# Performance work log

Hardware: AMD Instinct MI355X
Metric: run time of the kernel (lower is better)

The kernel has to match this reference:

```python
import jax, jax.numpy as jnp
import numpy as np

DIM = 1024
N_HEADS = 16
HEAD_DIM = DIM // N_HEADS


def setup_inputs() -> dict:
    key = jax.random.key(0)
    ks = jax.random.split(key, 9)
    s = 0.02
    return {
        "x": jax.random.normal(ks[0], (2, 2048, DIM), dtype=jnp.float32),
        "Wq": jax.random.normal(ks[1], (DIM, DIM), dtype=jnp.float32) * s,
        "bq": jax.random.normal(ks[2], (DIM,), dtype=jnp.float32) * s,
        "Wk": jax.random.normal(ks[3], (DIM, DIM), dtype=jnp.float32) * s,
        "bk": jax.random.normal(ks[4], (DIM,), dtype=jnp.float32) * s,
        "Wv": jax.random.normal(ks[5], (DIM, DIM), dtype=jnp.float32) * s,
        "bv": jax.random.normal(ks[6], (DIM,), dtype=jnp.float32) * s,
        "Wo": jax.random.normal(ks[7], (DIM, DIM), dtype=jnp.float32) * s,
        "bo": jax.random.normal(ks[8], (DIM,), dtype=jnp.float32) * s,
    }


def reference(x, Wq, bq, Wk, bk, Wv, bv, Wo, bo):
    B, T, C = x.shape
    # QKV projections, split heads -> [B, H, T, D]
    def split_heads(t):
        return t.reshape(B, T, N_HEADS, HEAD_DIM).transpose(0, 2, 1, 3)
    q = split_heads(x @ Wq + bq)
    k = split_heads(x @ Wk + bk)
    v = split_heads(x @ Wv + bv)
    scale = 1.0 / jnp.sqrt(jnp.float32(HEAD_DIM))
    scores = jnp.einsum("bhqd,bhkd->bhqk", q, k) * scale  # [B,H,T,T]
    causal = jnp.tril(jnp.ones((T, T), dtype=bool))  # True = keep
    scores = jnp.where(causal, scores, jnp.float32(-jnp.inf))
    weights = jax.nn.softmax(scores, axis=-1)
    ctx = jnp.einsum("bhqk,bhkd->bhqd", weights, v)
    ctx = ctx.transpose(0, 2, 1, 3).reshape(B, T, C)
    return ctx @ Wo + bo
```

## Files before the change

### kernel.cpp

```cpp
#include <hip/hip_runtime.h>
#include <hip/hip_bf16.h>
#include <stdint.h>

#define DIM    1024
#define SEQ    2048
#define NB     2
#define NH     16
#define HD     64
#define NROWS  (NB*SEQ)

typedef unsigned short u16;
typedef __attribute__((ext_vector_type(8))) short bf16x8;
typedef __attribute__((ext_vector_type(4))) float f32x4;
typedef __attribute__((ext_vector_type(4))) unsigned short u16x4;

#define NEG_INF (-__builtin_inff())

__device__ __forceinline__ u16 f2bf(float f) {
    union { float f; uint32_t u; } x; x.f = f;
    uint32_t r = x.u + 0x7FFFu + ((x.u >> 16) & 1u);
    return (u16)(r >> 16);
}

__device__ __forceinline__ uint32_t cvtpk(float a, float b) {
    uint32_t r;
    asm volatile("v_cvt_pk_bf16_f32 %0, %1, %2" : "=v"(r) : "v"(a), "v"(b));
    return r;
}

__device__ __forceinline__ void gload_lds16(const void* g, void* l) {
    __builtin_amdgcn_global_load_lds(
        (const __attribute__((address_space(1))) void*)g,
        (__attribute__((address_space(3))) void*)l, 16, 0, 0);
}

__global__ __launch_bounds__(256)
void cvt_x(const float* __restrict__ in, u16* __restrict__ out)
{
    size_t i = (size_t)blockIdx.x * 256 + threadIdx.x;
    float4 f = *(const float4*)&in[i * 4];
    u16x4 o = { f2bf(f.x), f2bf(f.y), f2bf(f.z), f2bf(f.w) };
    *(u16x4*)&out[i * 4] = o;
}

__global__ __launch_bounds__(256)
void cvt_w(const float* __restrict__ Wq, const float* __restrict__ Wk,
           const float* __restrict__ Wv, const float* __restrict__ Wo,
           u16* __restrict__ Wqt, u16* __restrict__ Wkt,
           u16* __restrict__ Wvt, u16* __restrict__ Wot)
{
    __shared__ u16 Ws[64][68];
    const int z = blockIdx.z;
    const float* W = z == 0 ? Wq : z == 1 ? Wk : z == 2 ? Wv : Wo;
    u16* Wt        = z == 0 ? Wqt : z == 1 ? Wkt : z == 2 ? Wvt : Wot;
    const int k0 = blockIdx.x * 64;
    const int n0 = blockIdx.y * 64;
    const int tid = threadIdx.x;

    #pragma unroll
    for (int it = 0; it < 4; ++it) {
        int idx = tid + it * 256;
        int r = idx >> 4, cq = idx & 15;
        float4 f = *(const float4*)&W[(size_t)(k0 + r) * DIM + n0 + cq * 4];
        u16x4 o = { f2bf(f.x), f2bf(f.y), f2bf(f.z), f2bf(f.w) };
        *(u16x4*)&Ws[r][cq * 4] = o;
    }
    __syncthreads();
    #pragma unroll
    for (int it = 0; it < 4; ++it) {
        int idx = tid + it * 256;
        int rr = idx >> 4, cq = idx & 15;
        u16x4 o = { Ws[cq*4+0][rr], Ws[cq*4+1][rr], Ws[cq*4+2][rr], Ws[cq*4+3][rr] };
        *(u16x4*)&Wt[(size_t)(n0 + rr) * DIM + k0 + cq * 4] = o;
    }
}

template<int MODE, int BN>
__global__ __launch_bounds__(256)
void gemm_mfma(const u16* __restrict__ A,
               const u16* __restrict__ Wt0, const u16* __restrict__ Wt1,
               const u16* __restrict__ Wt2,
               const float* __restrict__ b0, const float* __restrict__ b1,
               const float* __restrict__ b2,
               void* __restrict__ o0, void* __restrict__ o1, void* __restrict__ o2)
{
    constexpr int NJ = BN / 32;
    __shared__ __align__(16) uint8_t lds[16384 + BN * 128];
    uint8_t* Asb = lds;
    uint8_t* Bsb = lds + 16384;

    const int tid  = threadIdx.x;
    const int wid  = tid >> 6, lane = tid & 63;
    const int lr   = lane & 15, lg = lane >> 4;
    const int wr   = wid >> 1, wc = wid & 1;

    const int r0 = blockIdx.x * 128;
    const int c0 = blockIdx.y * BN;

    const u16* Wt; const float* bias; u16* obf = nullptr; float* ofp = nullptr;
    int cw; float qscale = 1.0f;
    if (MODE == 0) {
        int sel = c0 >> 10;
        cw  = c0 & 1023;
        Wt   = sel == 0 ? Wt0 : sel == 1 ? Wt1 : Wt2;
        bias = sel == 0 ? b0  : sel == 1 ? b1  : b2;
        obf  = (u16*)(sel == 0 ? o0 : sel == 1 ? o1 : o2);
        if (sel == 0) qscale = 0.125f * 1.44269504088896f;
    } else {
        cw = c0; Wt = Wt0; bias = b0; ofp = (float*)o0;
    }

    f32x4 acc[4][NJ] = {};

    for (int k0 = 0; k0 < DIM; k0 += 64) {
        __syncthreads();
        #pragma unroll
        for (int seg = 0; seg < 4; ++seg) {
            int o   = seg * 4096 + tid * 16;
            int row = o >> 7;
            int sch = ((o >> 4) & 7) ^ (row & 7);
            gload_lds16((const uint8_t*)A  + ((size_t)(r0 + row) << 11) + (k0 << 1) + (sch << 4),
                        Asb + seg * 4096 + (wid << 10) + (lane << 4));
            if (seg < BN / 32)
                gload_lds16((const uint8_t*)Wt + ((size_t)(cw + row) << 11) + (k0 << 1) + (sch << 4),
                            Bsb + seg * 4096 + (wid << 10) + (lane << 4));
        }
        __syncthreads();

        __builtin_amdgcn_s_setprio(1);
        #pragma unroll
        for (int kk = 0; kk < 2; ++kk) {
            bf16x8 a[4], b[NJ];
            #pragma unroll
            for (int i = 0; i < 4; ++i) {
                int ar = wr * 64 + i * 16 + lr;
                a[i] = *(const bf16x8*)(Asb + ar * 128 + ((((kk << 2) | lg) ^ (ar & 7)) << 4));
            }
            #pragma unroll
            for (int j = 0; j < NJ; ++j) {
                int br = wc * (BN / 2) + j * 16 + lr;
                b[j] = *(const bf16x8*)(Bsb + br * 128 + ((((kk << 2) | lg) ^ (br & 7)) << 4));
            }
            #pragma unroll
            for (int i = 0; i < 4; ++i)
                #pragma unroll
                for (int j = 0; j < NJ; ++j)
                    acc[i][j] = __builtin_amdgcn_mfma_f32_16x16x32_bf16(a[i], b[j], acc[i][j], 0, 0, 0);
        }
        __builtin_amdgcn_s_setprio(0);
    }

    #pragma unroll
    for (int j = 0; j < NJ; ++j) {
        int colw = wc * (BN / 2) + j * 16 + lr;
        float bv = bias[cw + colw];
        #pragma unroll
        for (int i = 0; i < 4; ++i) {
            #pragma unroll
            for (int r = 0; r < 4; ++r) {
                float val = (acc[i][j][r] + bv) * qscale;
                int row = r0 + wr * 64 + i * 16 + lg * 4 + r;
                if (MODE == 0) {
                    int col = cw + colw;
                    int h = col >> 6, d = col & 63;
                    int bb = row >> 11, t = row & (SEQ - 1);
                    obf[((((size_t)bb * NH + h) * SEQ + t) << 6) + d] = f2bf(val);
                } else {
                    ofp[((size_t)row << 10) + c0 + colw] = val;
                }
            }
        }
    }
}

template<int SPLIT>
__global__ __launch_bounds__(256)
void attn_mfma(const u16* __restrict__ q, const u16* __restrict__ k,
               const u16* __restrict__ v, u16* __restrict__ ctx,
               float* __restrict__ pO, float* __restrict__ pML)
{
    __shared__ __align__(16) uint8_t lds[16384];
    uint8_t* Ks = lds;
    uint8_t* Vt = lds + 8192;

    const int tid = threadIdx.x;
    const int wid = tid >> 6, lane = tid & 63;
    const int lr  = lane & 15, lg = lane >> 4;

    const int n = blockIdx.x;
    int bh, qt, k_lo, k_hi, pidx = 0;
    if (SPLIT) {
        bh = n & 31;
        int u = n >> 5;
        qt = u >> 1;
        int chunk = u & 1;
        int T = qt + 1, hh = (T + 1) >> 1;
        k_lo = chunk ? hh : 0;
        k_hi = chunk ? T : hh;
        pidx = (((bh << 5) | qt) << 1) | chunk;
    } else {
        int j4 = n >> 8, c = n & 255, ch = c >> 5;
        bh = c & 31;
        qt = (j4 == 0) ? ch : (j4 == 1) ? (15 - ch)
           : (j4 == 2) ? (16 + ch) : (31 - ch);
        k_lo = 0; k_hi = qt + 1;
    }

    const size_t hb = (size_t)bh * SEQ * HD;
    const int q0 = qt * 64;

    const u16* qrow = q + hb + ((size_t)(q0 + wid * 16 + lr) << 6);
    bf16x8 aQ0 = *(const bf16x8*)(qrow + lg * 8);
    bf16x8 aQ1 = *(const bf16x8*)(qrow + 32 + lg * 8);

    const int kr  = tid >> 2;
    const int kc0 = (tid & 3) * 2;
    const u16* kbase = k + hb + ((size_t)kr << 6) + kc0 * 8;

    const int vp = tid >> 3;
    const int vg = tid & 7;
    const int vj  = vp >> 3;
    const int vlg = (vp >> 1) & 3;
    const int vrr = (vp & 1) * 2;
    const int vslot = (vj & 1) * 32 + vlg * 8 + ((vj >> 1) << 2) + vrr;
    const u16* vbase = v + hb + ((size_t)(2 * vp) << 6) + vg * 8;

    bf16x8 kpre0 = {}, kpre1 = {}, vpre0 = {}, vpre1 = {};
    if (k_lo < k_hi) {
        const u16* ks = kbase + ((size_t)k_lo << 12);
        kpre0 = *(const bf16x8*)(ks);
        kpre1 = *(const bf16x8*)(ks + 8);
        const u16* vs = vbase + ((size_t)k_lo << 12);
        vpre0 = *(const bf16x8*)(vs);
        vpre1 = *(const bf16x8*)(vs + 64);
    }

    f32x4 acc[4] = {};
    float m_own = NEG_INF;
    float l_own = 0.f;

    for (int kt = k_lo; kt < k_hi; ++kt) {
        __syncthreads();
        *(bf16x8*)(Ks + kr * 128 + ((kc0       ^ (kr & 7)) << 4)) = kpre0;
        *(bf16x8*)(Ks + kr * 128 + (((kc0 + 1) ^ (kr & 7)) << 4)) = kpre1;
        #pragma unroll
        for (int i = 0; i < 8; ++i) {
            int d = vg * 8 + i;
            int swzd = (d ^ (d >> 3)) & 7;
            uint32_t w = (uint32_t)(u16)vpre0[i] | ((uint32_t)(u16)vpre1[i] << 16);
            *(uint32_t*)(Vt + d * 128 + ((((vslot >> 3) ^ swzd) << 4))
                         + ((vslot & 7) << 1)) = w;
        }
        __syncthreads();

        if (kt + 1 < k_hi) {
            const u16* ks = kbase + ((size_t)(kt + 1) << 12);
            kpre0 = *(const bf16x8*)(ks);
            kpre1 = *(const bf16x8*)(ks + 8);
            const u16* vs = vbase + ((size_t)(kt + 1) << 12);
            vpre0 = *(const bf16x8*)(vs);
            vpre1 = *(const bf16x8*)(vs + 64);
        }

        f32x4 s[4];
        __builtin_amdgcn_s_setprio(1);
        #pragma unroll
        for (int j = 0; j < 4; ++j) {
            int krow = j * 16 + lr;
            bf16x8 b0 = *(const bf16x8*)(Ks + krow * 128 + ((lg       ^ (krow & 7)) << 4));
            bf16x8 b1 = *(const bf16x8*)(Ks + krow * 128 + (((4 | lg) ^ (krow & 7)) << 4));
            f32x4 z = {0.f, 0.f, 0.f, 0.f};
            z    = __builtin_amdgcn_mfma_f32_16x16x32_bf16(b0, aQ0, z, 0, 0, 0);
            s[j] = __builtin_amdgcn_mfma_f32_16x16x32_bf16(b1, aQ1, z, 0, 0, 0);
        }
        __builtin_amdgcn_s_setprio(0);

        if (kt == qt) {
            #pragma unroll
            for (int j = 0; j < 4; ++j)
                #pragma unroll
                for (int r = 0; r < 4; ++r)
                    if (j * 16 + lg * 4 + r > wid * 16 + lr) s[j][r] = NEG_INF;
        }

        float rm = NEG_INF;
        #pragma unroll
        for (int j = 0; j < 4; ++j) {
            float a = fmaxf(fmaxf(s[j][0], s[j][1]), fmaxf(s[j][2], s[j][3]));
            rm = fmaxf(rm, a);
        }
        rm = fmaxf(rm, __shfl_xor(rm, 16));
        rm = fmaxf(rm, __shfl_xor(rm, 32));

        if (!__all(rm <= m_own + 8.f)) {
            float mnew = fmaxf(m_own, rm);
            float aown = exp2f(m_own - mnew);
            m_own = mnew;
            l_own *= aown;
            float ar[4];
            #pragma unroll
            for (int r = 0; r < 4; ++r) ar[r] = __shfl(aown, lg * 4 + r);
            #pragma unroll
            for (int ni = 0; ni < 4; ++ni)
                #pragma unroll
                for (int r = 0; r < 4; ++r)
                    acc[ni][r] *= ar[r];
        }

        float rs = 0.f;
        #pragma unroll
        for (int j = 0; j < 4; ++j)
            #pragma unroll
            for (int r = 0; r < 4; ++r) {
                float p = exp2f(s[j][r] - m_own);
                s[j][r] = p;
                rs += p;
            }
        rs += __shfl_xor(rs, 16);
        rs += __shfl_xor(rs, 32);
        l_own += rs;

        union { uint32_t u[4]; bf16x8 h; } P0, P1;
        P0.u[0] = cvtpk(s[0][0], s[0][1]); P0.u[1] = cvtpk(s[0][2], s[0][3]);
        P0.u[2] = cvtpk(s[2][0], s[2][1]); P0.u[3] = cvtpk(s[2][2], s[2][3]);
        P1.u[0] = cvtpk(s[1][0], s[1][1]); P1.u[1] = cvtpk(s[1][2], s[1][3]);
        P1.u[2] = cvtpk(s[3][0], s[3][1]); P1.u[3] = cvtpk(s[3][2], s[3][3]);

        __builtin_amdgcn_s_setprio(1);
        #pragma unroll
        for (int ni = 0; ni < 4; ++ni) {
            int vrow = ni * 16 + lr;
            int swzd = (vrow ^ (vrow >> 3)) & 7;
            bf16x8 vb0 = *(const bf16x8*)(Vt + vrow * 128 + ((lg       ^ swzd) << 4));
            bf16x8 vb1 = *(const bf16x8*)(Vt + vrow * 128 + (((4 | lg) ^ swzd) << 4));
            acc[ni] = __builtin_amdgcn_mfma_f32_16x16x32_bf16(P0.h, vb0, acc[ni], 0, 0, 0);
            acc[ni] = __builtin_amdgcn_mfma_f32_16x16x32_bf16(P1.h, vb1, acc[ni], 0, 0, 0);
        }
        __builtin_amdgcn_s_setprio(0);
    }

    if (SPLIT) {
        float* Op = pO + (size_t)pidx * 4096;
        #pragma unroll
        for (int r = 0; r < 4; ++r) {
            int row = wid * 16 + lg * 4 + r;
            #pragma unroll
            for (int ni = 0; ni < 4; ++ni)
                Op[row * 64 + ni * 16 + lr] = acc[ni][r];
        }
        if (lg == 0) {
            pML[pidx * 128 + wid * 16 + lr]      = m_own;
            pML[pidx * 128 + 64 + wid * 16 + lr] = l_own;
        }
    } else {
        float rinv = 1.f / l_own;
        float rl[4];
        #pragma unroll
        for (int r = 0; r < 4; ++r) rl[r] = __shfl(rinv, lg * 4 + r);
        const int b = bh >> 4, h = bh & 15;
        #pragma unroll
        for (int r = 0; r < 4; ++r) {
            int t = q0 + wid * 16 + lg * 4 + r;
            size_t base = (((size_t)b * SEQ + t) << 10) + (h << 6);
            #pragma unroll
            for (int ni = 0; ni < 4; ++ni)
                ctx[base + ni * 16 + lr] = f2bf(acc[ni][r] * rl[r]);
        }
    }
}

__global__ __launch_bounds__(256)
void attn_combine(const float* __restrict__ pO, const float* __restrict__ pML,
                  u16* __restrict__ ctx)
{
    int gid  = blockIdx.x * 256 + threadIdx.x;
    int rg   = gid >> 2;
    int dseg = gid & 3;
    int bh = rg >> 11;
    int qt = (rg >> 6) & 31;
    int r  = rg & 63;
    int p0 = ((bh << 5) | qt) << 1;

    float m0 = pML[p0 * 128 + r],       l0 = pML[p0 * 128 + 64 + r];
    float m1 = pML[(p0 + 1) * 128 + r], l1 = pML[(p0 + 1) * 128 + 64 + r];
    float m  = fmaxf(m0, m1);
    float s0 = exp2f(m0 - m), s1 = exp2f(m1 - m);
    float rl = 1.f / (l0 * s0 + l1 * s1);

    const float* O0 = pO + (size_t)p0 * 4096 + r * 64 + dseg * 16;
    const float* O1 = O0 + 4096;

    int b = bh >> 4, h = bh & 15, t = qt * 64 + r;
    u16* dst = ctx + (((size_t)b * SEQ + t) << 10) + (h << 6) + dseg * 16;

    u16x4 o[4];
    #pragma unroll
    for (int i = 0; i < 4; ++i) {
        float4 a = *(const float4*)&O0[i * 4];
        float4 c = *(const float4*)&O1[i * 4];
        o[i].x = f2bf((a.x * s0 + c.x * s1) * rl);
        o[i].y = f2bf((a.y * s0 + c.y * s1) * rl);
        o[i].z = f2bf((a.z * s0 + c.z * s1) * rl);
        o[i].w = f2bf((a.w * s0 + c.w * s1) * rl);
    }
    *(u16x4*)(dst)      = o[0];
    *(u16x4*)(dst + 4)  = o[1];
    *(u16x4*)(dst + 8)  = o[2];
    *(u16x4*)(dst + 12) = o[3];
}

extern "C" void kernel_launch(void* const* d_in, const int* in_sizes, int n_in,
                              void* d_out, int out_size, void* d_ws, size_t ws_size,
                              hipStream_t stream)
{
    (void)in_sizes; (void)n_in; (void)out_size;
    const float* x  = (const float*)d_in[0];
    const float* Wq = (const float*)d_in[1];
    const float* bq = (const float*)d_in[2];
    const float* Wk = (const float*)d_in[3];
    const float* bk = (const float*)d_in[4];
    const float* Wv = (const float*)d_in[5];
    const float* bv = (const float*)d_in[6];
    const float* Wo = (const float*)d_in[7];
    const float* bo = (const float*)d_in[8];

    u16* ws = (u16*)d_ws;
    const size_t M1 = (size_t)1024 * 1024;
    const size_t M4 = (size_t)NROWS * DIM;
    u16* xb  = ws;
    u16* wqt = ws + M4;
    u16* wkt = wqt + M1;
    u16* wvt = wkt + M1;
    u16* wot = wvt + M1;
    u16* qb  = wot + M1;
    u16* kb  = qb + M4;
    u16* vb  = kb + M4;
    u16* cb  = vb + M4;
    float* pO  = (float*)(cb + M4);
    float* pML = pO + (size_t)2048 * 4096;

    const size_t need = (size_t)(cb + M4 - ws) * 2
                      + (size_t)2048 * 4096 * 4 + (size_t)2048 * 128 * 4;
    const bool split = ws_size >= need;

    cvt_x<<<dim3(4096), dim3(256), 0, stream>>>(x, xb);
    cvt_w<<<dim3(16, 16, 4), dim3(256), 0, stream>>>(Wq, Wk, Wv, Wo, wqt, wkt, wvt, wot);
    gemm_mfma<0, 128><<<dim3(32, 24), dim3(256), 0, stream>>>(
        xb, wqt, wkt, wvt, bq, bk, bv, qb, kb, vb);
    if (split) {
        attn_mfma<1><<<dim3(2048), dim3(256), 0, stream>>>(qb, kb, vb, nullptr, pO, pML);
        attn_combine<<<dim3(1024), dim3(256), 0, stream>>>(pO, pML, cb);
    } else {
        attn_mfma<0><<<dim3(1024), dim3(256), 0, stream>>>(qb, kb, vb, cb, nullptr, nullptr);
    }
    gemm_mfma<1, 64><<<dim3(32, 16), dim3(256), 0, stream>>>(
        cb, wot, nullptr, nullptr, bo, nullptr, nullptr, d_out, nullptr, nullptr);
}
```

Measured before the change: 186.9 us.

## Use 128-row query tiles with 8 waves sharing each K/V tile in attention

The attention kernel now runs 512 threads (8 waves) per block and covers a 128-row query tile instead of 64. Each staged 64-key K/V tile is reused by twice as many query rows, which halves the global K/V traffic and the number of LDS staging passes per query. Each thread now loads half as much K/V per iteration. The causal mask is generalized to the two diagonal key tiles and uses a large finite negative value instead of -inf. The split partial-buffer layout and the combine kernel are rescaled to match. The costs are half as many blocks, the loss of the balanced block ordering in the non-split path, and more causal-mask waste on the diagonal.

```diff
diff --git a/kernel.cpp b/kernel.cpp
--- a/kernel.cpp
+++ b/kernel.cpp
@@ -11,10 +11,12 @@
 
 typedef unsigned short u16;
 typedef __attribute__((ext_vector_type(8))) short bf16x8;
+typedef __attribute__((ext_vector_type(4))) short bf16x4;
 typedef __attribute__((ext_vector_type(4))) float f32x4;
 typedef __attribute__((ext_vector_type(4))) unsigned short u16x4;
 
 #define NEG_INF (-__builtin_inff())
+#define MASK_NEG (-1.0e30f)
 
 __device__ __forceinline__ u16 f2bf(float f) {
     union { float f; uint32_t u; } x; x.f = f;
@@ -174,7 +176,7 @@
 }
 
 template<int SPLIT>
-__global__ __launch_bounds__(256)
+__global__ __launch_bounds__(512)
 void attn_mfma(const u16* __restrict__ q, const u16* __restrict__ k,
                const u16* __restrict__ v, u16* __restrict__ ctx,
                float* __restrict__ pO, float* __restrict__ pML)
@@ -188,51 +190,47 @@
     const int lr  = lane & 15, lg = lane >> 4;
 
     const int n = blockIdx.x;
-    int bh, qt, k_lo, k_hi, pidx = 0;
+    int bh, qtile, k_lo, k_hi, pidx = 0;
     if (SPLIT) {
         bh = n & 31;
         int u = n >> 5;
-        qt = u >> 1;
+        qtile = u >> 1;
         int chunk = u & 1;
-        int T = qt + 1, hh = (T + 1) >> 1;
+        int T = 2 * qtile + 2, hh = qtile + 1;
         k_lo = chunk ? hh : 0;
         k_hi = chunk ? T : hh;
-        pidx = (((bh << 5) | qt) << 1) | chunk;
+        pidx = (((bh << 4) | qtile) << 1) | chunk;
     } else {
-        int j4 = n >> 8, c = n & 255, ch = c >> 5;
-        bh = c & 31;
-        qt = (j4 == 0) ? ch : (j4 == 1) ? (15 - ch)
-           : (j4 == 2) ? (16 + ch) : (31 - ch);
-        k_lo = 0; k_hi = qt + 1;
+        qtile = n >> 5; bh = n & 31;
+        k_lo = 0; k_hi = 2 * qtile + 2;
     }
 
     const size_t hb = (size_t)bh * SEQ * HD;
-    const int q0 = qt * 64;
+    const int q0 = qtile << 7;
 
     const u16* qrow = q + hb + ((size_t)(q0 + wid * 16 + lr) << 6);
     bf16x8 aQ0 = *(const bf16x8*)(qrow + lg * 8);
     bf16x8 aQ1 = *(const bf16x8*)(qrow + 32 + lg * 8);
 
-    const int kr  = tid >> 2;
-    const int kc0 = (tid & 3) * 2;
-    const u16* kbase = k + hb + ((size_t)kr << 6) + kc0 * 8;
-
-    const int vp = tid >> 3;
-    const int vg = tid & 7;
+    const int kr = tid >> 3;
+    const int kc = tid & 7;
+    const u16* kbase = k + hb + ((size_t)kr << 6) + kc * 8;
+
+    const int vp = tid >> 4;
+    const int dg = tid & 15;
     const int vj  = vp >> 3;
     const int vlg = (vp >> 1) & 3;
     const int vrr = (vp & 1) * 2;
     const int vslot = (vj & 1) * 32 + vlg * 8 + ((vj >> 1) << 2) + vrr;
-    const u16* vbase = v + hb + ((size_t)(2 * vp) << 6) + vg * 8;
-
-    bf16x8 kpre0 = {}, kpre1 = {}, vpre0 = {}, vpre1 = {};
+    const u16* vbase = v + hb + ((size_t)(2 * vp) << 6) + dg * 4;
+
+    bf16x8 kpre = {};
+    bf16x4 vpre0 = {}, vpre1 = {};
     if (k_lo < k_hi) {
-        const u16* ks = kbase + ((size_t)k_lo << 12);
-        kpre0 = *(const bf16x8*)(ks);
-        kpre1 = *(const bf16x8*)(ks + 8);
+        kpre  = *(const bf16x8*)(kbase + ((size_t)k_lo << 12));
         const u16* vs = vbase + ((size_t)k_lo << 12);
-        vpre0 = *(const bf16x8*)(vs);
-        vpre1 = *(const bf16x8*)(vs + 64);
+        vpre0 = *(const bf16x4*)(vs);
+        vpre1 = *(const bf16x4*)(vs + 64);
     }
 
     f32x4 acc[4] = {};
@@ -241,11 +239,10 @@
 
     for (int kt = k_lo; kt < k_hi; ++kt) {
         __syncthreads();
-        *(bf16x8*)(Ks + kr * 128 + ((kc0       ^ (kr & 7)) << 4)) = kpre0;
-        *(bf16x8*)(Ks + kr * 128 + (((kc0 + 1) ^ (kr & 7)) << 4)) = kpre1;
-        #pragma unroll
-        for (int i = 0; i < 8; ++i) {
-            int d = vg * 8 + i;
+        *(bf16x8*)(Ks + kr * 128 + ((kc ^ (kr & 7)) << 4)) = kpre;
+        #pragma unroll
+        for (int i = 0; i < 4; ++i) {
+            int d = dg * 4 + i;
             int swzd = (d ^ (d >> 3)) & 7;
             uint32_t w = (uint32_t)(u16)vpre0[i] | ((uint32_t)(u16)vpre1[i] << 16);
             *(uint32_t*)(Vt + d * 128 + ((((vslot >> 3) ^ swzd) << 4))
@@ -254,12 +251,10 @@
         __syncthreads();
 
         if (kt + 1 < k_hi) {
-            const u16* ks = kbase + ((size_t)(kt + 1) << 12);
-            kpre0 = *(const bf16x8*)(ks);
-            kpre1 = *(const bf16x8*)(ks + 8);
+            kpre  = *(const bf16x8*)(kbase + ((size_t)(kt + 1) << 12));
             const u16* vs = vbase + ((size_t)(kt + 1) << 12);
-            vpre0 = *(const bf16x8*)(vs);
-            vpre1 = *(const bf16x8*)(vs + 64);
+            vpre0 = *(const bf16x4*)(vs);
+            vpre1 = *(const bf16x4*)(vs + 64);
         }
 
         f32x4 s[4];
@@ -275,12 +270,13 @@
         }
         __builtin_amdgcn_s_setprio(0);
 
-        if (kt == qt) {
+        if (((kt + 1) << 6) > q0) {
             #pragma unroll
             for (int j = 0; j < 4; ++j)
                 #pragma unroll
                 for (int r = 0; r < 4; ++r)
-                    if (j * 16 + lg * 4 + r > wid * 16 + lr) s[j][r] = NEG_INF;
+                    if ((kt << 6) + j * 16 + lg * 4 + r > q0 + wid * 16 + lr)
+                        s[j][r] = MASK_NEG;
         }
 
         float rm = NEG_INF;
@@ -340,7 +336,7 @@
     }
 
     if (SPLIT) {
-        float* Op = pO + (size_t)pidx * 4096;
+        float* Op = pO + (size_t)pidx * 8192;
         #pragma unroll
         for (int r = 0; r < 4; ++r) {
             int row = wid * 16 + lg * 4 + r;
@@ -349,8 +345,8 @@
                 Op[row * 64 + ni * 16 + lr] = acc[ni][r];
         }
         if (lg == 0) {
-            pML[pidx * 128 + wid * 16 + lr]      = m_own;
-            pML[pidx * 128 + 64 + wid * 16 + lr] = l_own;
+            pML[pidx * 256 + wid * 16 + lr]       = m_own;
+            pML[pidx * 256 + 128 + wid * 16 + lr] = l_own;
         }
     } else {
         float rinv = 1.f / l_own;
@@ -376,21 +372,21 @@
     int gid  = blockIdx.x * 256 + threadIdx.x;
     int rg   = gid >> 2;
     int dseg = gid & 3;
-    int bh = rg >> 11;
-    int qt = (rg >> 6) & 31;
-    int r  = rg & 63;
-    int p0 = ((bh << 5) | qt) << 1;
-
-    float m0 = pML[p0 * 128 + r],       l0 = pML[p0 * 128 + 64 + r];
-    float m1 = pML[(p0 + 1) * 128 + r], l1 = pML[(p0 + 1) * 128 + 64 + r];
+    int bh    = rg >> 11;
+    int qtile = (rg >> 7) & 15;
+    int r     = rg & 127;
+    int p0 = ((bh << 4) | qtile) << 1;
+
+    float m0 = pML[p0 * 256 + r],       l0 = pML[p0 * 256 + 128 + r];
+    float m1 = pML[(p0 + 1) * 256 + r], l1 = pML[(p0 + 1) * 256 + 128 + r];
     float m  = fmaxf(m0, m1);
     float s0 = exp2f(m0 - m), s1 = exp2f(m1 - m);
     float rl = 1.f / (l0 * s0 + l1 * s1);
 
-    const float* O0 = pO + (size_t)p0 * 4096 + r * 64 + dseg * 16;
-    const float* O1 = O0 + 4096;
-
-    int b = bh >> 4, h = bh & 15, t = qt * 64 + r;
+    const float* O0 = pO + (size_t)p0 * 8192 + r * 64 + dseg * 16;
+    const float* O1 = O0 + 8192;
+
+    int b = bh >> 4, h = bh & 15, t = qtile * 128 + r;
     u16* dst = ctx + (((size_t)b * SEQ + t) << 10) + (h << 6) + dseg * 16;
 
     u16x4 o[4];
@@ -437,10 +433,10 @@
     u16* vb  = kb + M4;
     u16* cb  = vb + M4;
     float* pO  = (float*)(cb + M4);
-    float* pML = pO + (size_t)2048 * 4096;
+    float* pML = pO + (size_t)1024 * 8192;
 
     const size_t need = (size_t)(cb + M4 - ws) * 2
-                      + (size_t)2048 * 4096 * 4 + (size_t)2048 * 128 * 4;
+                      + (size_t)1024 * 8192 * 4 + (size_t)1024 * 256 * 4;
     const bool split = ws_size >= need;
 
     cvt_x<<<dim3(4096), dim3(256), 0, stream>>>(x, xb);
@@ -448,10 +444,10 @@
     gemm_mfma<0, 128><<<dim3(32, 24), dim3(256), 0, stream>>>(
         xb, wqt, wkt, wvt, bq, bk, bv, qb, kb, vb);
     if (split) {
-        attn_mfma<1><<<dim3(2048), dim3(256), 0, stream>>>(qb, kb, vb, nullptr, pO, pML);
+        attn_mfma<1><<<dim3(1024), dim3(512), 0, stream>>>(qb, kb, vb, nullptr, pO, pML);
         attn_combine<<<dim3(1024), dim3(256), 0, stream>>>(pO, pML, cb);
     } else {
-        attn_mfma<0><<<dim3(1024), dim3(256), 0, stream>>>(qb, kb, vb, cb, nullptr, nullptr);
+        attn_mfma<0><<<dim3(512), dim3(512), 0, stream>>>(qb, kb, vb, cb, nullptr, nullptr);
     }
     gemm_mfma<1, 64><<<dim3(32, 16), dim3(256), 0, stream>>>(
         cb, wot, nullptr, nullptr, bo, nullptr, nullptr, d_out, nullptr, nullptr);
```

New measurement: 190.9 us. +2.1%, slower.
